# Optimization experiments

Measured on AMD Instinct MI355X. Metric: run time of the kernel, lower is better.

## Reference

```python
import jax, jax.numpy as jnp
import numpy as np

B, D, N, M = 8, 256, 2048, 2048
H = 4
DH = D // H  # 64
EPS = 1e-5


def setup_inputs() -> dict:
    key = jax.random.key(0)
    ks = jax.random.split(key, 16)
    s = 0.05
    return {
        "x": jax.random.normal(ks[0], (B, D, N), jnp.float32),
        "source": jax.random.normal(ks[1], (B, D, M), jnp.float32),
        # per-head QKV projection weights (equivalent to H separate Conv1d(D, DH, 1))
        "Wq": jax.random.normal(ks[2], (H, DH, D), jnp.float32) * s,
        "bq": jax.random.normal(ks[3], (H, DH), jnp.float32) * s,
        "Wk": jax.random.normal(ks[4], (H, DH, D), jnp.float32) * s,
        "bk": jax.random.normal(ks[5], (H, DH), jnp.float32) * s,
        "Wv": jax.random.normal(ks[6], (H, DH, D), jnp.float32) * s,
        "bv": jax.random.normal(ks[7], (H, DH), jnp.float32) * s,
        # merge Conv1d(D, D, 1)
        "Wm": jax.random.normal(ks[8], (D, D), jnp.float32) * s,
        "bm": jax.random.normal(ks[9], (D,), jnp.float32) * s,
        # MLP: Conv1d(2D, 2D, 1) -> InstanceNorm -> ReLU -> Conv1d(2D, D, 1)
        "W1": jax.random.normal(ks[10], (2 * D, 2 * D), jnp.float32) * s,
        "b1": jax.random.normal(ks[11], (2 * D,), jnp.float32) * s,
        "W2": jax.random.normal(ks[12], (D, 2 * D), jnp.float32) * s,
        "b2": jnp.zeros((D,), jnp.float32),  # nn.init.constant_(mlp[-1].bias, 0.0)
    }


def reference(x, source, Wq, bq, Wk, bk, Wv, bv, Wm, bm, W1, b1, W2, b2):
    # Per-head 1x1-conv QKV projections, batched: [B, DH, H, N]
    q = jnp.einsum('bdn,hkd->bkhn', x, Wq) + bq.T[None, :, :, None]
    k = jnp.einsum('bdm,hkd->bkhm', source, Wk) + bk.T[None, :, :, None]
    v = jnp.einsum('bdm,hkd->bkhm', source, Wv) + bv.T[None, :, :, None]
    # scaled dot-product attention (scale = head dim)
    scores = jnp.einsum('bkhn,bkhm->bhnm', q, k) / jnp.sqrt(jnp.float32(DH))
    prob = jax.nn.softmax(scores, axis=-1)
    msg = jnp.einsum('bhnm,bkhm->bkhn', prob, v)
    # view(B, DH*H, N): dim-major then head, matches jnp reshape of [B, DH, H, N]
    msg = msg.reshape(B, DH * H, N)
    message = jnp.einsum('bcn,ec->ben', msg, Wm) + bm[None, :, None]
    # MLP on concat([x, message])
    h = jnp.concatenate([x, message], axis=1)  # [B, 2D, N]
    h = jnp.einsum('bcn,oc->bon', h, W1) + b1[None, :, None]
    # InstanceNorm1d (affine=False, biased variance, eps=1e-5) over N per (b, c)
    mean = jnp.mean(h, axis=-1, keepdims=True)
    var = jnp.var(h, axis=-1, keepdims=True)
    h = (h - mean) / jnp.sqrt(var + EPS)
    h = jax.nn.relu(h)
    out = jnp.einsum('bcn,oc->bon', h, W2) + b2[None, :, None]
    return out
```

## Files before the change

kernel.cpp:

```cpp
#include <hip/hip_runtime.h>
#include <hip/hip_bf16.h>

#define B_  8
#define D_  256
#define N_  2048
#define M_  2048
#define H_  4
#define DH_ 64
#define D2_ 512

#define SCL_QK 0.1803368801f

typedef unsigned short ushort_t;
typedef __attribute__((ext_vector_type(8))) short bf16x8;
typedef __attribute__((ext_vector_type(4))) short bf16x4;
typedef __attribute__((ext_vector_type(4))) float f32x4;

__device__ __forceinline__ unsigned cvtpk(float a, float b) {
  unsigned r;
  asm("v_cvt_pk_bf16_f32 %0, %1, %2" : "=v"(r) : "v"(a), "v"(b));
  return r;
}
__device__ __forceinline__ ushort_t f2bf1(float x) {
  return (ushort_t)cvtpk(x, x);
}
__device__ __forceinline__ float bf2f(ushort_t h) {
  union { unsigned u; float f; } c; c.u = ((unsigned)h) << 16; return c.f;
}
__device__ __forceinline__ uint2 pack4(float a, float b, float c, float d) {
  uint2 r; r.x = cvtpk(a, b); r.y = cvtpk(c, d); return r;
}

template <int K, int LDB>
__device__ __forceinline__ void mfma_core(const ushort_t* __restrict__ Arow,
                                          const ushort_t* __restrict__ Brow,
                                          f32x4 acc[4][4], int lg) {
#pragma unroll 2
  for (int k0 = 0; k0 < K; k0 += 32) {
    bf16x8 af[4], bfr[4];
#pragma unroll
    for (int f = 0; f < 4; ++f)
      af[f] = *(const bf16x8*)&Arow[(size_t)16 * f * K + k0 + lg * 8];
#pragma unroll
    for (int f = 0; f < 4; ++f)
      bfr[f] = *(const bf16x8*)&Brow[(size_t)16 * f * LDB + k0 + lg * 8];
#pragma unroll
    for (int fm = 0; fm < 4; ++fm)
#pragma unroll
      for (int fn = 0; fn < 4; ++fn)
        acc[fm][fn] = __builtin_amdgcn_mfma_f32_16x16x32_bf16(
            af[fm], bfr[fn], acc[fm][fn], 0, 0, 0);
  }
}

#define GEMM_PREAMBLE()                                   \
  const int t = threadIdx.x, lane = t & 63, wv = t >> 6;  \
  const int wm = wv >> 1, wn = wv & 1;                    \
  const int lq = lane & 15, lg = lane >> 4;               \
  const int m0 = blockIdx.y * 128 + wm * 64;              \
  const int n0 = blockIdx.x * 128 + wn * 64;              \
  f32x4 acc[4][4];                                        \
  _Pragma("unroll") for (int i = 0; i < 4; ++i)           \
  _Pragma("unroll") for (int j = 0; j < 4; ++j)           \
      acc[i][j] = (f32x4){0.f, 0.f, 0.f, 0.f};

__global__ __launch_bounds__(256) void prep_weights(
    const float* __restrict__ Wq, const float* __restrict__ Wk,
    const float* __restrict__ Wv, const float* __restrict__ Wm,
    const float* __restrict__ W1, const float* __restrict__ W2,
    ushort_t* __restrict__ Wqb, ushort_t* __restrict__ Wkb,
    ushort_t* __restrict__ Wvb, ushort_t* __restrict__ Wmb,
    ushort_t* __restrict__ W1b, ushort_t* __restrict__ W2b) {
  const int idx = blockIdx.x * 256 + threadIdx.x;
  if (idx < 65536) {
    Wqb[idx] = f2bf1(Wq[idx] * SCL_QK);
  } else if (idx < 131072) {
    int j = idx - 65536; Wkb[j] = f2bf1(Wk[j]);
  } else if (idx < 196608) {
    int j = idx - 131072; Wvb[j] = f2bf1(Wv[j]);
  } else if (idx < 262144) {
    int j = idx - 196608;
    int e = j >> 8, cp = j & 255;
    int h = cp >> 6, dh = cp & 63;
    Wmb[j] = f2bf1(Wm[e * 256 + dh * 4 + h]);
  } else if (idx < 524288) {
    int j = idx - 262144; W1b[j] = f2bf1(W1[j]);
  } else if (idx < 655360) {
    int j = idx - 524288; W2b[j] = f2bf1(W2[j]);
  }
}

__global__ __launch_bounds__(256) void transpose_in(
    const float* __restrict__ x, const float* __restrict__ source,
    ushort_t* __restrict__ cat_t, ushort_t* __restrict__ st) {
  __shared__ float T[64][65];
  const int t = threadIdx.x;
  const int b = blockIdx.z & 7, which = blockIdx.z >> 3;
  const float* sb = (which ? source : x) + (size_t)b * D_ * N_;
  ushort_t* dst = which ? st + (size_t)b * N_ * 256 : cat_t + (size_t)b * N_ * 512;
  const int ldc = which ? 256 : 512;
  const int d0 = blockIdx.y * 64, n0 = blockIdx.x * 64;
  const int nn = t & 63, dd = t >> 6;
#pragma unroll
  for (int p = 0; p < 16; ++p)
    T[dd + 4 * p][nn] = sb[(size_t)(d0 + dd + 4 * p) * N_ + n0 + nn];
  __syncthreads();
  const int dg = t & 7, nr = t >> 3;
#pragma unroll
  for (int p = 0; p < 2; ++p) {
    int n = nr + 32 * p;
    uint4 pv;
    pv.x = cvtpk(T[dg * 8 + 0][n], T[dg * 8 + 1][n]);
    pv.y = cvtpk(T[dg * 8 + 2][n], T[dg * 8 + 3][n]);
    pv.z = cvtpk(T[dg * 8 + 4][n], T[dg * 8 + 5][n]);
    pv.w = cvtpk(T[dg * 8 + 6][n], T[dg * 8 + 7][n]);
    *(uint4*)&dst[(size_t)(n0 + n) * ldc + d0 + dg * 8] = pv;
  }
}

__global__ __launch_bounds__(256) void q_mfma(
    const ushort_t* __restrict__ Wqb, const float* __restrict__ bq,
    const ushort_t* __restrict__ cat_t, ushort_t* __restrict__ Qt) {
  GEMM_PREAMBLE()
  const int b = blockIdx.z;
  const ushort_t* Arow = Wqb + (size_t)(m0 + lq) * 256;
  const ushort_t* Brow = cat_t + ((size_t)b * N_ + n0 + lq) * 512;
  mfma_core<256, 512>(Arow, Brow, acc, lg);
  ushort_t* Qb = Qt + (size_t)b * 4 * N_ * 64;
#pragma unroll
  for (int fm = 0; fm < 4; ++fm) {
    const int o0 = m0 + 16 * fm + 4 * lg;
    const int hh = o0 >> 6, dl = o0 & 63;
    float bb[4];
#pragma unroll
    for (int r = 0; r < 4; ++r) bb[r] = bq[o0 + r] * SCL_QK;
#pragma unroll
    for (int fn = 0; fn < 4; ++fn) {
      const int n = n0 + 16 * fn + lq;
      uint2 pv = pack4(acc[fm][fn][0] + bb[0], acc[fm][fn][1] + bb[1],
                       acc[fm][fn][2] + bb[2], acc[fm][fn][3] + bb[3]);
      *(uint2*)&Qb[((size_t)hh * N_ + n) * 64 + dl] = pv;
    }
  }
}

__global__ __launch_bounds__(256) void kv_mfma(
    const ushort_t* __restrict__ Wkb, const ushort_t* __restrict__ Wvb,
    const float* __restrict__ bk, const float* __restrict__ bv,
    const ushort_t* __restrict__ st, ushort_t* __restrict__ Kt,
    ushort_t* __restrict__ Vt) {
  const int b = blockIdx.z >> 1, w = blockIdx.z & 1;
  GEMM_PREAMBLE()
  const ushort_t* A = w ? Wvb : Wkb;
  const float* bias = w ? bv : bk;
  const ushort_t* Arow = A + (size_t)(m0 + lq) * 256;
  const ushort_t* Brow = st + ((size_t)b * N_ + n0 + lq) * 256;
  mfma_core<256, 256>(Arow, Brow, acc, lg);
  if (w == 0) {
    ushort_t* Kb = Kt + (size_t)b * 4 * N_ * 64;
#pragma unroll
    for (int fm = 0; fm < 4; ++fm) {
      const int o0 = m0 + 16 * fm + 4 * lg;
      const int hh = o0 >> 6, dl = o0 & 63;
      float bb[4];
#pragma unroll
      for (int r = 0; r < 4; ++r) bb[r] = bias[o0 + r];
#pragma unroll
      for (int fn = 0; fn < 4; ++fn) {
        const int n = n0 + 16 * fn + lq;
        uint2 pv = pack4(acc[fm][fn][0] + bb[0], acc[fm][fn][1] + bb[1],
                         acc[fm][fn][2] + bb[2], acc[fm][fn][3] + bb[3]);
        *(uint2*)&Kb[((size_t)hh * N_ + n) * 64 + dl] = pv;
      }
    }
  } else {
    ushort_t* Vb = Vt + (size_t)b * 256 * N_;
#pragma unroll
    for (int fm = 0; fm < 4; ++fm) {
      const int o0 = m0 + 16 * fm + 4 * lg;
      float bb[4];
#pragma unroll
      for (int r = 0; r < 4; ++r) bb[r] = bias[o0 + r];
#pragma unroll
      for (int fn = 0; fn < 4; ++fn) {
        const int n = n0 + 16 * fn + lq;
#pragma unroll
        for (int r = 0; r < 4; ++r)
          Vb[(size_t)(o0 + r) * N_ + n] = f2bf1(acc[fm][fn][r] + bb[r]);
      }
    }
  }
}

__global__ __launch_bounds__(256) void attn_mfma(
    const ushort_t* __restrict__ Qt, const ushort_t* __restrict__ Kt,
    const ushort_t* __restrict__ Vt, ushort_t* __restrict__ msgT) {
  __shared__ __align__(16) ushort_t Ks[64 * 64];
  __shared__ __align__(16) ushort_t Vs[80 * 64];
  __shared__ __align__(16) ushort_t Ps[64 * 64];
  const int t = threadIdx.x;
  const int lane = t & 63, wq = t >> 6;
  const int flat = blockIdx.x;
  const int logical = (flat & 7) * 128 + (flat >> 3);
  const int qt = logical & 31, h = (logical >> 5) & 3, b = logical >> 7;
  const int bh = b * H_ + h;
  const size_t base = (size_t)bh * 64 * N_;
  const int n00 = qt * 64;
  const int lq = lane & 15, lg = lane >> 4;
  const int qrow = wq * 16 + lq;
  const int sw = (lq & 7) * 8;

  {
    const int row = 64 + (t >> 4);
    const int c4 = (t & 15) * 4;
    const unsigned fill = (row == 64) ? 0x3F803F80u : 0u;
    uint2 iv; iv.x = fill; iv.y = fill;
    *(uint2*)&Vs[row * 64 + c4] = iv;
  }

  bf16x8 qf0, qf1;
  {
    const ushort_t* qp = Qt + base + (size_t)(n00 + qrow) * 64 + lg * 8;
    qf0 = *(const bf16x8*)qp;
    qf1 = *(const bf16x8*)(qp + 32);
  }
  f32x4 o0 = {0.f, 0.f, 0.f, 0.f}, o1 = o0, o2 = o0, o3 = o0, l4 = o0;
  const int sdg = (t & 7) * 8, srw = t >> 3;

  for (int m0 = 0; m0 < M_; m0 += 64) {
#pragma unroll
    for (int p = 0; p < 2; ++p) {
      int r = srw + 32 * p;
      int wsw = (r & 7) * 8;
      *(bf16x8*)&Ks[r * 64 + (sdg ^ wsw)] =
          *(const bf16x8*)(Kt + base + (size_t)(m0 + r) * 64 + sdg);
      *(bf16x8*)&Vs[r * 64 + (sdg ^ wsw)] =
          *(const bf16x8*)(Vt + base + (size_t)r * N_ + m0 + sdg);
    }
    __syncthreads();

    f32x4 s0 = {0.f, 0.f, 0.f, 0.f}, s1 = s0, s2 = s0, s3 = s0;
#pragma unroll
    for (int kt = 0; kt < 2; ++kt) {
      const int dh0 = (lg * 8 + 32 * kt) ^ sw;
      const bf16x8 qb = kt ? qf1 : qf0;
      s0 = __builtin_amdgcn_mfma_f32_16x16x32_bf16(
          *(const bf16x8*)&Ks[lq * 64 + dh0], qb, s0, 0, 0, 0);
      s1 = __builtin_amdgcn_mfma_f32_16x16x32_bf16(
          *(const bf16x8*)&Ks[(16 + lq) * 64 + dh0], qb, s1, 0, 0, 0);
      s2 = __builtin_amdgcn_mfma_f32_16x16x32_bf16(
          *(const bf16x8*)&Ks[(32 + lq) * 64 + dh0], qb, s2, 0, 0, 0);
      s3 = __builtin_amdgcn_mfma_f32_16x16x32_bf16(
          *(const bf16x8*)&Ks[(48 + lq) * 64 + dh0], qb, s3, 0, 0, 0);
    }

#define PSTORE(SF, KF)                                                    \
    {                                                                     \
      uint2 pv;                                                           \
      pv.x = cvtpk(exp2f(SF[0]), exp2f(SF[1]));                           \
      pv.y = cvtpk(exp2f(SF[2]), exp2f(SF[3]));                           \
      *(uint2*)&Ps[qrow * 64 + ((16 * (KF) + 4 * lg) ^ sw)] = pv;         \
    }
    PSTORE(s0, 0) PSTORE(s1, 1) PSTORE(s2, 2) PSTORE(s3, 3)
#undef PSTORE
    asm volatile("s_waitcnt lgkmcnt(0)" ::: "memory");

#pragma unroll
    for (int kt = 0; kt < 2; ++kt) {
      const int k0 = (lg * 8 + 32 * kt) ^ sw;
      const bf16x8 pb = *(const bf16x8*)&Ps[qrow * 64 + k0];
      o0 = __builtin_amdgcn_mfma_f32_16x16x32_bf16(
          *(const bf16x8*)&Vs[lq * 64 + k0], pb, o0, 0, 0, 0);
      o1 = __builtin_amdgcn_mfma_f32_16x16x32_bf16(
          *(const bf16x8*)&Vs[(16 + lq) * 64 + k0], pb, o1, 0, 0, 0);
      o2 = __builtin_amdgcn_mfma_f32_16x16x32_bf16(
          *(const bf16x8*)&Vs[(32 + lq) * 64 + k0], pb, o2, 0, 0, 0);
      o3 = __builtin_amdgcn_mfma_f32_16x16x32_bf16(
          *(const bf16x8*)&Vs[(48 + lq) * 64 + k0], pb, o3, 0, 0, 0);
      l4 = __builtin_amdgcn_mfma_f32_16x16x32_bf16(
          *(const bf16x8*)&Vs[(64 + lq) * 64 + k0], pb, l4, 0, 0, 0);
    }
    __syncthreads();
  }

  const float lsum = __shfl(l4[0], lq);
  const float inv = 1.f / lsum;

  ushort_t* mp = msgT + ((size_t)b * N_ + n00 + qrow) * 256 + h * 64;
  uint2 pv;
  pv = pack4(o0[0] * inv, o0[1] * inv, o0[2] * inv, o0[3] * inv);
  *(uint2*)&mp[0 + 4 * lg] = pv;
  pv = pack4(o1[0] * inv, o1[1] * inv, o1[2] * inv, o1[3] * inv);
  *(uint2*)&mp[16 + 4 * lg] = pv;
  pv = pack4(o2[0] * inv, o2[1] * inv, o2[2] * inv, o2[3] * inv);
  *(uint2*)&mp[32 + 4 * lg] = pv;
  pv = pack4(o3[0] * inv, o3[1] * inv, o3[2] * inv, o3[3] * inv);
  *(uint2*)&mp[48 + 4 * lg] = pv;
}

__global__ __launch_bounds__(256) void merge_mfma(
    const ushort_t* __restrict__ Wmb, const float* __restrict__ bm,
    const ushort_t* __restrict__ msgT, ushort_t* __restrict__ cat_t) {
  GEMM_PREAMBLE()
  const int b = blockIdx.z;
  const ushort_t* Arow = Wmb + (size_t)(m0 + lq) * 256;
  const ushort_t* Brow = msgT + ((size_t)b * N_ + n0 + lq) * 256;
  mfma_core<256, 256>(Arow, Brow, acc, lg);
  ushort_t* ob = cat_t + (size_t)b * N_ * 512 + 256;
#pragma unroll
  for (int fm = 0; fm < 4; ++fm) {
    const int o0 = m0 + 16 * fm + 4 * lg;
    float bb[4];
#pragma unroll
    for (int r = 0; r < 4; ++r) bb[r] = bm[o0 + r];
#pragma unroll
    for (int fn = 0; fn < 4; ++fn) {
      const int n = n0 + 16 * fn + lq;
      uint2 pv = pack4(acc[fm][fn][0] + bb[0], acc[fm][fn][1] + bb[1],
                       acc[fm][fn][2] + bb[2], acc[fm][fn][3] + bb[3]);
      *(uint2*)&ob[(size_t)n * 512 + o0] = pv;
    }
  }
}

__global__ __launch_bounds__(256) void w1_mfma(
    const ushort_t* __restrict__ W1b, const float* __restrict__ b1,
    const ushort_t* __restrict__ cat_t, ushort_t* __restrict__ h1t) {
  GEMM_PREAMBLE()
  const int b = blockIdx.z;
  const ushort_t* Arow = W1b + (size_t)(m0 + lq) * 512;
  const ushort_t* Brow = cat_t + ((size_t)b * N_ + n0 + lq) * 512;
  mfma_core<512, 512>(Arow, Brow, acc, lg);
  ushort_t* ob = h1t + (size_t)b * N_ * 512;
#pragma unroll
  for (int fm = 0; fm < 4; ++fm) {
    const int o0 = m0 + 16 * fm + 4 * lg;
    float bb[4];
#pragma unroll
    for (int r = 0; r < 4; ++r) bb[r] = b1[o0 + r];
#pragma unroll
    for (int fn = 0; fn < 4; ++fn) {
      const int n = n0 + 16 * fn + lq;
      uint2 pv = pack4(acc[fm][fn][0] + bb[0], acc[fm][fn][1] + bb[1],
                       acc[fm][fn][2] + bb[2], acc[fm][fn][3] + bb[3]);
      *(uint2*)&ob[(size_t)n * 512 + o0] = pv;
    }
  }
}

__global__ __launch_bounds__(256) void zero_stats(float* __restrict__ s) {
  s[blockIdx.x * 256 + threadIdx.x] = 0.f;
}

__global__ __launch_bounds__(256) void stats_partial(
    const ushort_t* __restrict__ h1t, float* __restrict__ ssum,
    float* __restrict__ ssq) {
  const int t = threadIdx.x;
  const int c = blockIdx.y * 64 + (t & 63);
  const int b = blockIdx.z;
  const int nbase = blockIdx.x * 256 + (t >> 6) * 64;
  const ushort_t* p = h1t + (size_t)b * N_ * 512;
  float s = 0.f, ss = 0.f;
  for (int i = 0; i < 64; ++i) {
    float v = bf2f(p[(size_t)(nbase + i) * 512 + c]);
    s += v; ss += v * v;
  }
  __shared__ float rs[4][64], rq[4][64];
  const int wv = t >> 6;
  rs[wv][t & 63] = s; rq[wv][t & 63] = ss;
  __syncthreads();
  if (t < 64) {
    float S = rs[0][t] + rs[1][t] + rs[2][t] + rs[3][t];
    float Q = rq[0][t] + rq[1][t] + rq[2][t] + rq[3][t];
    atomicAdd(&ssum[b * 512 + blockIdx.y * 64 + t], S);
    atomicAdd(&ssq[b * 512 + blockIdx.y * 64 + t], Q);
  }
}

__global__ __launch_bounds__(256) void finalize_stats(
    const float* __restrict__ ssum, const float* __restrict__ ssq,
    float* __restrict__ mean, float* __restrict__ istd) {
  const int i = blockIdx.x * 256 + threadIdx.x;
  float mn = ssum[i] * (1.f / N_);
  float var = ssq[i] * (1.f / N_) - mn * mn;
  mean[i] = mn;
  istd[i] = rsqrtf(var + 1e-5f);
}

__global__ __launch_bounds__(256) void normalize_h1(
    const ushort_t* __restrict__ h1t, const float* __restrict__ mean,
    const float* __restrict__ istd, ushort_t* __restrict__ h1n) {
  const size_t ci = (size_t)blockIdx.x * 256 + threadIdx.x;
  const size_t basei = ci * 8;
  const int c0 = (int)(basei & 511);
  const size_t row = basei >> 9;
  const int b = (int)(row >> 11);
  const float* mp = mean + b * 512 + c0;
  const float* ip = istd + b * 512 + c0;
  union { bf16x8 v; ushort_t u[8]; } in;
  in.v = *(const bf16x8*)&h1t[basei];
  float g[8];
#pragma unroll
  for (int j = 0; j < 8; ++j)
    g[j] = fmaxf((bf2f(in.u[j]) - mp[j]) * ip[j], 0.f);
  uint4 pv;
  pv.x = cvtpk(g[0], g[1]);
  pv.y = cvtpk(g[2], g[3]);
  pv.z = cvtpk(g[4], g[5]);
  pv.w = cvtpk(g[6], g[7]);
  *(uint4*)&h1n[basei] = pv;
}

__global__ __launch_bounds__(256) void w2_mfma(
    const ushort_t* __restrict__ W2b, const float* __restrict__ b2,
    const ushort_t* __restrict__ h1n, float* __restrict__ out) {
  GEMM_PREAMBLE()
  const int b = blockIdx.z;
  const ushort_t* Arow = W2b + (size_t)(m0 + lq) * 512;
  const ushort_t* Brow = h1n + ((size_t)b * N_ + n0 + lq) * 512;
  mfma_core<512, 512>(Arow, Brow, acc, lg);
  float* ob = out + (size_t)b * D_ * N_;
#pragma unroll
  for (int fm = 0; fm < 4; ++fm) {
    const int o0 = m0 + 16 * fm + 4 * lg;
    float bb[4];
#pragma unroll
    for (int r = 0; r < 4; ++r) bb[r] = b2[o0 + r];
#pragma unroll
    for (int fn = 0; fn < 4; ++fn) {
      const int n = n0 + 16 * fn + lq;
#pragma unroll
      for (int r = 0; r < 4; ++r)
        ob[(size_t)(o0 + r) * N_ + n] = acc[fm][fn][r] + bb[r];
    }
  }
}

extern "C" void kernel_launch(void* const* d_in, const int* in_sizes, int n_in,
                              void* d_out, int out_size, void* d_ws,
                              size_t ws_size, hipStream_t stream) {
  const float* x = (const float*)d_in[0];
  const float* source = (const float*)d_in[1];
  const float* Wq = (const float*)d_in[2];
  const float* bq = (const float*)d_in[3];
  const float* Wk = (const float*)d_in[4];
  const float* bk = (const float*)d_in[5];
  const float* Wv = (const float*)d_in[6];
  const float* bv = (const float*)d_in[7];
  const float* Wm = (const float*)d_in[8];
  const float* bm = (const float*)d_in[9];
  const float* W1 = (const float*)d_in[10];
  const float* b1 = (const float*)d_in[11];
  const float* W2 = (const float*)d_in[12];
  const float* b2 = (const float*)d_in[13];
  float* out = (float*)d_out;

  char* w = (char*)d_ws;
  size_t off = 0;
  auto alloc = [&](size_t bytes) {
    void* p = w + off;
    off = (off + bytes + 255) & ~(size_t)255;
    return p;
  };
  ushort_t* cat_t = (ushort_t*)alloc((size_t)B_ * N_ * 512 * 2);
  ushort_t* st    = (ushort_t*)alloc((size_t)B_ * N_ * 256 * 2);
  ushort_t* Qt    = (ushort_t*)alloc((size_t)B_ * 4 * N_ * 64 * 2);
  ushort_t* Kt    = (ushort_t*)alloc((size_t)B_ * 4 * N_ * 64 * 2);
  ushort_t* Vt    = (ushort_t*)alloc((size_t)B_ * 256 * N_ * 2);
  ushort_t* msgT  = (ushort_t*)alloc((size_t)B_ * N_ * 256 * 2);
  ushort_t* h1t   = (ushort_t*)alloc((size_t)B_ * N_ * 512 * 2);
  ushort_t* h1n   = (ushort_t*)alloc((size_t)B_ * N_ * 512 * 2);
  float* ssum = (float*)alloc(4096 * 4);
  float* ssq  = (float*)alloc(4096 * 4);
  float* mean = (float*)alloc(4096 * 4);
  float* istd = (float*)alloc(4096 * 4);
  ushort_t* Wqb = (ushort_t*)alloc(65536 * 2);
  ushort_t* Wkb = (ushort_t*)alloc(65536 * 2);
  ushort_t* Wvb = (ushort_t*)alloc(65536 * 2);
  ushort_t* Wmb = (ushort_t*)alloc(65536 * 2);
  ushort_t* W1b = (ushort_t*)alloc(262144 * 2);
  ushort_t* W2b = (ushort_t*)alloc(131072 * 2);

  prep_weights<<<2560, 256, 0, stream>>>(Wq, Wk, Wv, Wm, W1, W2, Wqb, Wkb,
                                         Wvb, Wmb, W1b, W2b);
  transpose_in<<<dim3(32, 4, 16), 256, 0, stream>>>(x, source, cat_t, st);
  zero_stats<<<32, 256, 0, stream>>>(ssum);
  q_mfma<<<dim3(16, 2, 8), 256, 0, stream>>>(Wqb, bq, cat_t, Qt);
  kv_mfma<<<dim3(16, 2, 16), 256, 0, stream>>>(Wkb, Wvb, bk, bv, st, Kt, Vt);
  attn_mfma<<<dim3(1024), 256, 0, stream>>>(Qt, Kt, Vt, msgT);
  merge_mfma<<<dim3(16, 2, 8), 256, 0, stream>>>(Wmb, bm, msgT, cat_t);
  w1_mfma<<<dim3(16, 4, 8), 256, 0, stream>>>(W1b, b1, cat_t, h1t);
  stats_partial<<<dim3(8, 8, 8), 256, 0, stream>>>(h1t, ssum, ssq);
  finalize_stats<<<16, 256, 0, stream>>>(ssum, ssq, mean, istd);
  normalize_h1<<<4096, 256, 0, stream>>>(h1t, mean, istd, h1n);
  w2_mfma<<<dim3(16, 2, 8), 256, 0, stream>>>(W2b, b2, h1n, out);
}
```

Baseline: 300.6 us.

## Double-buffer K/V tiles via async global-to-LDS loads and compute row sums in registers

The attention kernel now stages K and V tiles with global_load_lds direct-to-LDS loads into two ping-pong buffers, so the next tile is prefetched while the current one is used. This takes the global load latency off the critical path and drops the register round trip. The softmax denominator is now summed in registers from the fp32 exponentials and reduced across lanes with shuffles, replacing the extra ones-row MFMA on the V tile. LDS use grows from the second buffer, which may reduce occupancy, and the loop relies on a single barrier per tile to order the buffer reuse.

```diff
diff --git a/kernel.cpp b/kernel.cpp
--- a/kernel.cpp
+++ b/kernel.cpp
@@ -29,6 +29,12 @@
 }
 __device__ __forceinline__ uint2 pack4(float a, float b, float c, float d) {
   uint2 r; r.x = cvtpk(a, b); r.y = cvtpk(c, d); return r;
+}
+
+__device__ __forceinline__ void gload16(const ushort_t* g, ushort_t* l) {
+  __builtin_amdgcn_global_load_lds(
+      (const __attribute__((address_space(1))) unsigned*)g,
+      (__attribute__((address_space(3))) unsigned*)l, 16, 0, 0);
 }
 
 template <int K, int LDB>
@@ -195,8 +201,8 @@
 __global__ __launch_bounds__(256) void attn_mfma(
     const ushort_t* __restrict__ Qt, const ushort_t* __restrict__ Kt,
     const ushort_t* __restrict__ Vt, ushort_t* __restrict__ msgT) {
-  __shared__ __align__(16) ushort_t Ks[64 * 64];
-  __shared__ __align__(16) ushort_t Vs[80 * 64];
+  __shared__ __align__(16) ushort_t Ks[2 * 64 * 64];
+  __shared__ __align__(16) ushort_t Vs[2 * 64 * 64];
   __shared__ __align__(16) ushort_t Ps[64 * 64];
   const int t = threadIdx.x;
   const int lane = t & 63, wq = t >> 6;
@@ -210,13 +216,14 @@
   const int qrow = wq * 16 + lq;
   const int sw = (lq & 7) * 8;
 
-  {
-    const int row = 64 + (t >> 4);
-    const int c4 = (t & 15) * 4;
-    const unsigned fill = (row == 64) ? 0x3F803F80u : 0u;
-    uint2 iv; iv.x = fill; iv.y = fill;
-    *(uint2*)&Vs[row * 64 + c4] = iv;
-  }
+  const int r0 = wq * 16 + (lane >> 3);
+  const int r1 = r0 + 8;
+  const int c8 = lane & 7;
+  const ushort_t* kp0 = Kt + base + (size_t)r0 * 64 + ((c8 ^ (r0 & 7)) * 8);
+  const ushort_t* kp1 = Kt + base + (size_t)r1 * 64 + ((c8 ^ (r1 & 7)) * 8);
+  const ushort_t* vp0 = Vt + base + (size_t)r0 * N_ + ((c8 ^ (r0 & 7)) * 8);
+  const ushort_t* vp1 = Vt + base + (size_t)r1 * N_ + ((c8 ^ (r1 & 7)) * 8);
+  const int wbase = wq * 1024;
 
   bf16x8 qf0, qf1;
   {
@@ -224,25 +231,32 @@
     qf0 = *(const bf16x8*)qp;
     qf1 = *(const bf16x8*)(qp + 32);
   }
-  f32x4 o0 = {0.f, 0.f, 0.f, 0.f}, o1 = o0, o2 = o0, o3 = o0, l4 = o0;
-  const int sdg = (t & 7) * 8, srw = t >> 3;
-
-  for (int m0 = 0; m0 < M_; m0 += 64) {
-#pragma unroll
-    for (int p = 0; p < 2; ++p) {
-      int r = srw + 32 * p;
-      int wsw = (r & 7) * 8;
-      *(bf16x8*)&Ks[r * 64 + (sdg ^ wsw)] =
-          *(const bf16x8*)(Kt + base + (size_t)(m0 + r) * 64 + sdg);
-      *(bf16x8*)&Vs[r * 64 + (sdg ^ wsw)] =
-          *(const bf16x8*)(Vt + base + (size_t)r * N_ + m0 + sdg);
-    }
-    __syncthreads();
+  f32x4 o0 = {0.f, 0.f, 0.f, 0.f}, o1 = o0, o2 = o0, o3 = o0;
+  float lrun = 0.f;
+
+  gload16(kp0, &Ks[wbase]);
+  gload16(kp1, &Ks[wbase + 512]);
+  gload16(vp0, &Vs[wbase]);
+  gload16(vp1, &Vs[wbase + 512]);
+  kp0 += 4096; kp1 += 4096; vp0 += 64; vp1 += 64;
+  __syncthreads();
+
+  int cur = 0;
+  for (int tile = 0; tile < 32; ++tile) {
+    if (tile != 31) {
+      const int nb = (cur ^ 1) * 4096;
+      gload16(kp0, &Ks[nb + wbase]);
+      gload16(kp1, &Ks[nb + wbase + 512]);
+      gload16(vp0, &Vs[nb + wbase]);
+      gload16(vp1, &Vs[nb + wbase + 512]);
+      kp0 += 4096; kp1 += 4096; vp0 += 64; vp1 += 64;
+    }
+    const int kb = cur * 4096;
 
     f32x4 s0 = {0.f, 0.f, 0.f, 0.f}, s1 = s0, s2 = s0, s3 = s0;
 #pragma unroll
     for (int kt = 0; kt < 2; ++kt) {
-      const int dh0 = (lg * 8 + 32 * kt) ^ sw;
+      const int dh0 = ((lg * 8 + 32 * kt) ^ sw) + kb;
       const bf16x8 qb = kt ? qf1 : qf0;
       s0 = __builtin_amdgcn_mfma_f32_16x16x32_bf16(
           *(const bf16x8*)&Ks[lq * 64 + dh0], qb, s0, 0, 0, 0);
@@ -254,37 +268,43 @@
           *(const bf16x8*)&Ks[(48 + lq) * 64 + dh0], qb, s3, 0, 0, 0);
     }
 
+    float ls = 0.f;
 #define PSTORE(SF, KF)                                                    \
     {                                                                     \
+      float e0 = exp2f(SF[0]), e1 = exp2f(SF[1]);                         \
+      float e2 = exp2f(SF[2]), e3 = exp2f(SF[3]);                         \
+      ls += (e0 + e1) + (e2 + e3);                                        \
       uint2 pv;                                                           \
-      pv.x = cvtpk(exp2f(SF[0]), exp2f(SF[1]));                           \
-      pv.y = cvtpk(exp2f(SF[2]), exp2f(SF[3]));                           \
+      pv.x = cvtpk(e0, e1);                                               \
+      pv.y = cvtpk(e2, e3);                                               \
       *(uint2*)&Ps[qrow * 64 + ((16 * (KF) + 4 * lg) ^ sw)] = pv;         \
     }
     PSTORE(s0, 0) PSTORE(s1, 1) PSTORE(s2, 2) PSTORE(s3, 3)
 #undef PSTORE
+    lrun += ls;
     asm volatile("s_waitcnt lgkmcnt(0)" ::: "memory");
+    __builtin_amdgcn_sched_barrier(0);
 
 #pragma unroll
     for (int kt = 0; kt < 2; ++kt) {
       const int k0 = (lg * 8 + 32 * kt) ^ sw;
       const bf16x8 pb = *(const bf16x8*)&Ps[qrow * 64 + k0];
       o0 = __builtin_amdgcn_mfma_f32_16x16x32_bf16(
-          *(const bf16x8*)&Vs[lq * 64 + k0], pb, o0, 0, 0, 0);
+          *(const bf16x8*)&Vs[lq * 64 + k0 + kb], pb, o0, 0, 0, 0);
       o1 = __builtin_amdgcn_mfma_f32_16x16x32_bf16(
-          *(const bf16x8*)&Vs[(16 + lq) * 64 + k0], pb, o1, 0, 0, 0);
+          *(const bf16x8*)&Vs[(16 + lq) * 64 + k0 + kb], pb, o1, 0, 0, 0);
       o2 = __builtin_amdgcn_mfma_f32_16x16x32_bf16(
-          *(const bf16x8*)&Vs[(32 + lq) * 64 + k0], pb, o2, 0, 0, 0);
+          *(const bf16x8*)&Vs[(32 + lq) * 64 + k0 + kb], pb, o2, 0, 0, 0);
       o3 = __builtin_amdgcn_mfma_f32_16x16x32_bf16(
-          *(const bf16x8*)&Vs[(48 + lq) * 64 + k0], pb, o3, 0, 0, 0);
-      l4 = __builtin_amdgcn_mfma_f32_16x16x32_bf16(
-          *(const bf16x8*)&Vs[(64 + lq) * 64 + k0], pb, l4, 0, 0, 0);
+          *(const bf16x8*)&Vs[(48 + lq) * 64 + k0 + kb], pb, o3, 0, 0, 0);
     }
     __syncthreads();
-  }
-
-  const float lsum = __shfl(l4[0], lq);
-  const float inv = 1.f / lsum;
+    cur ^= 1;
+  }
+
+  lrun += __shfl_xor(lrun, 16);
+  lrun += __shfl_xor(lrun, 32);
+  const float inv = 1.f / lrun;
 
   ushort_t* mp = msgT + ((size_t)b * N_ + n00 + qrow) * 256 + h * 64;
   uint2 pv;
```

New measurement: 286.9 us. 1.05x faster.
